# Optimization experiments

Hardware: AMD Instinct MI355X
Metric: run time of the kernel (lower is better)

## Reference

```python
import jax, jax.numpy as jnp
import numpy as np

NUM_RELATIONS = 16


def rgcn_conv(x, src, dst, etype, W, root, b):
    """PyG-style RGCNConv: per-relation mean aggregation + root weight + bias.

    x: [N, din]; W: [R, din, dout]; root: [din, dout]; b: [dout].
    """
    N, din = x.shape
    R = W.shape[0]
    E = src.shape[0]
    xe = x[src]                                   # [E, din] gather
    seg = etype * N + dst                          # combined (relation, dst) key
    sums = jax.ops.segment_sum(xe, seg, num_segments=R * N)        # [R*N, din]
    cnt = jax.ops.segment_sum(jnp.ones((E,), x.dtype), seg, num_segments=R * N)
    mean = (sums / jnp.maximum(cnt, 1.0)[:, None]).reshape(R, N, din)
    # mean-then-transform == PyG transform-then-mean (linearity)
    out = jnp.einsum('rnd,rde->ne', mean, W) + x @ root + b
    return out


def setup_inputs() -> dict:
    key = jax.random.key(0)
    ks = jax.random.split(key, 8)
    N, E, DIN, H, OUT, R = 40000, 640000, 386, 256, 2, NUM_RELATIONS
    x = jax.random.normal(ks[0], (N, DIN), dtype=jnp.float32)
    edge_index = jax.random.randint(ks[1], (2, E), 0, N, dtype=jnp.int64)
    edge_type = jax.random.randint(ks[2], (E,), 0, R, dtype=jnp.int64)
    s1 = 1.0 / np.sqrt(DIN)
    s2 = 1.0 / np.sqrt(H)
    W1 = jax.random.normal(ks[3], (R, DIN, H), dtype=jnp.float32) * s1
    root1 = jax.random.normal(ks[4], (DIN, H), dtype=jnp.float32) * s1
    b1 = jnp.zeros((H,), dtype=jnp.float32)
    W2 = jax.random.normal(ks[5], (R, H, OUT), dtype=jnp.float32) * s2
    root2 = jax.random.normal(ks[6], (H, OUT), dtype=jnp.float32) * s2
    b2 = jnp.zeros((OUT,), dtype=jnp.float32)
    return {"x": x, "edge_index": edge_index, "edge_type": edge_type,
            "W1": W1, "root1": root1, "b1": b1,
            "W2": W2, "root2": root2, "b2": b2}


def reference(x, edge_index, edge_type, W1, root1, b1, W2, root2, b2):
    src, dst = edge_index[0], edge_index[1]
    h = jax.nn.relu(rgcn_conv(x, src, dst, edge_type, W1, root1, b1))
    h = rgcn_conv(h, src, dst, edge_type, W2, root2, b2)
    return jnp.tanh(h)
```

## Files before the change

### kernel.cpp

```cpp
#include <hip/hip_runtime.h>
#include <cstdint>
#include <cstddef>

#define N_NODES 40000
#define DIN     386
#define H1      256
#define NREL    16
#define KPAD    416
#define MPAD    40064
#define NMT     313
#define NBREL   16
#define NCOL1   ((NREL + 1) * H1)
#define Y2C     (2 * NREL + 2)
#define N2PAD   48
#define LDB2    264
#define NWPR    625
#define ROWCAP  26112
#define NMTCP   208
#define NSB     40
#define NXB     8138
#define NB1B    7072
#define NB2B    48

typedef __attribute__((ext_vector_type(8))) short s8v;
typedef __attribute__((ext_vector_type(4))) float f4v;

__device__ __forceinline__ uint16_t f2h(float f) {
  _Float16 h = (_Float16)f;
  return *(uint16_t*)&h;
}
__device__ __forceinline__ float h2f(uint16_t u) {
  _Float16 h = *(_Float16*)&u;
  return (float)h;
}
__device__ __forceinline__ f4v mfma_f16(s8v a, s8v b, f4v c) {
  asm("v_mfma_f32_16x16x32_f16 %0, %1, %2, %0" : "+v"(c) : "v"(a), "v"(b));
  return c;
}
__device__ __forceinline__ void gload16(const uint16_t* g, const uint16_t* lds) {
  __builtin_amdgcn_global_load_lds(
      (const __attribute__((address_space(1))) unsigned int*)g,
      (__attribute__((address_space(3))) unsigned int*)lds, 16, 0, 0);
}

__global__ void k_count(const int* __restrict__ src, const int* __restrict__ dst,
                        const int* __restrict__ et, int* __restrict__ deg,
                        uint8_t* __restrict__ flagS, int* __restrict__ epos, int E) {
  int e = blockIdx.x * 256 + threadIdx.x;
  if (e < E) {
    epos[e] = atomicAdd(&deg[dst[e]], 1);
    flagS[et[e] * N_NODES + src[e]] = 1;
  }
}

__global__ void k_wcount(const uint8_t* __restrict__ flagS, int* __restrict__ wcnt) {
  int i = blockIdx.x * 256 + threadIdx.x;
  unsigned long long m = __ballot(flagS[i] != 0);
  if ((threadIdx.x & 63) == 0) wcnt[i >> 6] = (int)__popcll(m);
}

__global__ void k_scan1(const int* __restrict__ wcnt, int* __restrict__ wbase,
                        int* __restrict__ nsrc, const int* __restrict__ deg,
                        int* __restrict__ rowptr, int* __restrict__ bsum) {
  __shared__ int sd[1024];
  int t = threadIdx.x;
  if (blockIdx.x < NREL) {
    int r = blockIdx.x;
    int v = (t < NWPR) ? wcnt[r * NWPR + t] : 0;
    sd[t] = v;
    __syncthreads();
    for (int off = 1; off < 1024; off <<= 1) {
      int x = (t >= off) ? sd[t - off] : 0;
      __syncthreads();
      sd[t] += x;
      __syncthreads();
    }
    if (t < NWPR) wbase[r * NWPR + t] = sd[t] - v;
    if (t == NWPR - 1) nsrc[r] = sd[t];
  } else {
    int b = blockIdx.x - NREL;
    int i = b * 1024 + t;
    int v = (i < N_NODES) ? deg[i] : 0;
    sd[t] = v;
    __syncthreads();
    for (int off = 1; off < 1024; off <<= 1) {
      int x = (t >= off) ? sd[t - off] : 0;
      __syncthreads();
      sd[t] += x;
      __syncthreads();
    }
    if (i < N_NODES) rowptr[i + 1] = sd[t];
    if (t == 1023) bsum[b] = sd[t];
  }
}

__global__ void k_assign(const uint8_t* __restrict__ flagS,
                         const int* __restrict__ wbase,
                         int* __restrict__ posmap, int* __restrict__ srclist) {
  int i = blockIdx.x * 256 + threadIdx.x;
  int lane = threadIdx.x & 63;
  bool act = flagS[i] != 0;
  unsigned long long m = __ballot(act);
  if (act) {
    int pre = (int)__popcll(m & ((1ULL << lane) - 1));
    int p = wbase[i >> 6] + pre;
    int r = i / N_NODES, s = i - r * N_NODES;
    if (p < ROWCAP) {
      posmap[i] = p;
      srclist[r * ROWCAP + p] = s;
    } else {
      posmap[i] = ROWCAP - 1;
    }
  }
}

__global__ void k_s3(const int* __restrict__ bsum, int* __restrict__ rowptr) {
  __shared__ int s_off;
  int b = blockIdx.x, t = threadIdx.x;
  if (t < 64) {
    int lane = t;
    int v = (lane < NSB) ? bsum[lane] : 0;
    for (int o = 1; o < 64; o <<= 1) {
      int x = __shfl_up(v, o);
      if (lane >= o) v += x;
    }
    int off = (b == 0) ? 0 : __shfl(v, b - 1);
    if (lane == 0) s_off = off;
  }
  __syncthreads();
  int off = s_off;
  int i = b * 1024 + t;
  if (i < N_NODES && b > 0) rowptr[i + 1] += off;
  if (b == 0 && t == 0) rowptr[0] = 0;
}

__global__ void k_scatter(const int* __restrict__ src, const int* __restrict__ dst,
                          const int* __restrict__ et, const int* __restrict__ rowptr,
                          const int* __restrict__ epos, const int* __restrict__ posmap,
                          int* __restrict__ e_rp, int* __restrict__ e_rs, int E) {
  int e = blockIdx.x * 256 + threadIdx.x;
  if (e < E) {
    int d = dst[e], r = et[e], s = src[e];
    int idx = rowptr[d] + epos[e];
    e_rp[idx] = (r << 16) | posmap[r * N_NODES + s];
    e_rs[idx] = (r << 16) | s;
  }
}

__global__ void k_pack(const float* __restrict__ x, const float* __restrict__ W1,
                       const float* __restrict__ root1, const float* __restrict__ W2,
                       const float* __restrict__ root2, uint16_t* __restrict__ xh,
                       uint16_t* __restrict__ b1h, uint16_t* __restrict__ b2h) {
  int bb = blockIdx.x;
  int tid = threadIdx.x;
  if (bb < NXB) {
    long long i = (long long)bb * 256 + tid;
    if (i >= (long long)MPAD * (KPAD / 8)) return;
    int n = (int)(i / (KPAD / 8)), kv = (int)(i % (KPAD / 8));
    int k = kv * 8;
    uint4 o = {0u, 0u, 0u, 0u};
    if (n < N_NODES) {
      const float* xr = x + (long long)n * DIN;
      if (k + 8 <= DIN) {
        float2 p0 = *(const float2*)(xr + k);
        float2 p1 = *(const float2*)(xr + k + 2);
        float2 p2 = *(const float2*)(xr + k + 4);
        float2 p3 = *(const float2*)(xr + k + 6);
        o.x = (uint32_t)f2h(p0.x) | ((uint32_t)f2h(p0.y) << 16);
        o.y = (uint32_t)f2h(p1.x) | ((uint32_t)f2h(p1.y) << 16);
        o.z = (uint32_t)f2h(p2.x) | ((uint32_t)f2h(p2.y) << 16);
        o.w = (uint32_t)f2h(p3.x) | ((uint32_t)f2h(p3.y) << 16);
      } else if (k < DIN) {
        uint16_t t[8];
#pragma unroll
        for (int j = 0; j < 8; ++j) t[j] = (k + j < DIN) ? f2h(xr[k + j]) : 0;
        o.x = (uint32_t)t[0] | ((uint32_t)t[1] << 16);
        o.y = (uint32_t)t[2] | ((uint32_t)t[3] << 16);
        o.z = (uint32_t)t[4] | ((uint32_t)t[5] << 16);
        o.w = (uint32_t)t[6] | ((uint32_t)t[7] << 16);
      }
    }
    *(uint4*)(xh + (long long)n * KPAD + k) = o;
  } else if (bb < NXB + NB1B) {
    long long i = (long long)(bb - NXB) * 256 + tid;
    int c = (int)(i / KPAD), k = (int)(i % KPAD);
    float v = 0.0f;
    if (k < DIN) {
      if (c < NREL * H1) {
        int r = c >> 8, j = c & 255;
        v = W1[((long long)r * DIN + k) * H1 + j];
      } else {
        v = root1[(long long)k * H1 + (c - NREL * H1)];
      }
    }
    b1h[i] = f2h(v);
  } else {
    int i = (bb - NXB - NB1B) * 256 + tid;
    int c = i >> 8, k = i & 255;
    float v = 0.0f;
    if (c < 2 * NREL) { int r = c >> 1, j = c & 1; v = W2[(r * H1 + k) * 2 + j]; }
    else if (c < Y2C) v = root2[k * 2 + (c - 2 * NREL)];
    b2h[i] = f2h(v);
  }
}

__global__ __launch_bounds__(256) void k_gemm1(
    const uint16_t* __restrict__ A, const uint16_t* __restrict__ B,
    const uint16_t* __restrict__ Broot, uint16_t* __restrict__ C,
    uint16_t* __restrict__ h, int ldc, int nb, int jrel,
    const int* __restrict__ srclist, const int* __restrict__ nsrc, int r0) {
  __shared__ __align__(16) uint16_t sA[2][128 * 32];
  __shared__ __align__(16) uint16_t sB[2][256 * 32];
  int tid = threadIdx.x;
  int lane = tid & 63, w = tid >> 6;
  int wr = w >> 1, wcn = w & 1;

  int f = blockIdx.x;
  int xcd = f & 7, j = f >> 3;
  bool root = (j >= jrel);
  int mt, yt = 0, ns;
  const uint16_t* Bp;
  long long bn = 0;
  if (!root) {
    yt = j % nb;
    mt = (j / nb) * 8 + xcd;
    ns = nsrc[r0 + yt];
    if (ns > ROWCAP) ns = ROWCAP;
    Bp = B;
    bn = (long long)yt * 256;
  } else {
    mt = (j - jrel) * 8 + xcd;
    if (mt >= NMT) return;
    ns = N_NODES;
    Bp = Broot;
  }
  long long bm = (long long)mt * 128;
  if (bm >= ns) return;

  int lrow = lane & 15;
  int lko = (((lane >> 4) ^ ((lane >> 1) & 3)) * 8);

  int arow = tid >> 2;
  int skel = (((tid & 3) ^ ((tid >> 3) & 3)) * 8);

  long long rowA0, rowA1;
  if (!root) {
    const int* sl = srclist + (r0 + yt) * ROWCAP;
    int ia = (int)bm + arow, ib = ia + 64;
    rowA0 = sl[ia < ns ? ia : 0];
    rowA1 = sl[ib < ns ? ib : 0];
  } else {
    rowA0 = bm + arow;
    rowA1 = bm + arow + 64;
  }

  const uint16_t* gA0 = A + rowA0 * KPAD + skel;
  const uint16_t* gA1 = A + rowA1 * KPAD + skel;
  const uint16_t* gB0 = Bp + (bn + arow) * KPAD + skel;
  const uint16_t* gB1 = gB0 + (long long)64 * KPAD;
  const uint16_t* gB2 = gB0 + (long long)128 * KPAD;
  const uint16_t* gB3 = gB0 + (long long)192 * KPAD;

  f4v zero = {0.f, 0.f, 0.f, 0.f};
  f4v acc[4][8];
#pragma unroll
  for (int i = 0; i < 4; ++i)
#pragma unroll
    for (int jj = 0; jj < 8; ++jj) acc[i][jj] = zero;

  gload16(gA0, sA[0] + w * 512);
  gload16(gA1, sA[0] + 2048 + w * 512);
  gload16(gB0, sB[0] + w * 512);
  gload16(gB1, sB[0] + 2048 + w * 512);
  gload16(gB2, sB[0] + 4096 + w * 512);
  gload16(gB3, sB[0] + 6144 + w * 512);

  const int NIT = KPAD / 32;
  int cur = 0;
  for (int it = 0; it < NIT; ++it) {
    if (it + 1 < NIT) {
      int kk = (it + 1) * 32;
      int nxt = cur ^ 1;
      gload16(gA0 + kk, sA[nxt] + w * 512);
      gload16(gA1 + kk, sA[nxt] + 2048 + w * 512);
      gload16(gB0 + kk, sB[nxt] + w * 512);
      gload16(gB1 + kk, sB[nxt] + 2048 + w * 512);
      gload16(gB2 + kk, sB[nxt] + 4096 + w * 512);
      gload16(gB3 + kk, sB[nxt] + 6144 + w * 512);
      asm volatile("s_waitcnt vmcnt(6)" ::: "memory");
    } else {
      asm volatile("s_waitcnt vmcnt(0)" ::: "memory");
    }
    __builtin_amdgcn_s_barrier();

    const uint16_t* pA = sA[cur];
    const uint16_t* pB = sB[cur];
    s8v af[4];
#pragma unroll
    for (int mi = 0; mi < 4; ++mi)
      af[mi] = *(const s8v*)(pA + (wr * 64 + mi * 16 + lrow) * 32 + lko);
#pragma unroll
    for (int ni = 0; ni < 8; ++ni) {
      s8v bf = *(const s8v*)(pB + (wcn * 128 + ni * 16 + lrow) * 32 + lko);
#pragma unroll
      for (int mi = 0; mi < 4; ++mi)
        acc[mi][ni] = mfma_f16(af[mi], bf, acc[mi][ni]);
    }
    __builtin_amdgcn_s_barrier();
    cur ^= 1;
  }

  int rg = (lane >> 4) * 4;
  if (!root) {
#pragma unroll
    for (int mi = 0; mi < 4; ++mi) {
#pragma unroll
      for (int ni = 0; ni < 8; ++ni) {
        long long col = bn + wcn * 128 + ni * 16 + (lane & 15);
#pragma unroll
        for (int r2 = 0; r2 < 4; ++r2) {
          long long row = bm + wr * 64 + mi * 16 + rg + r2;
          C[row * ldc + col] = f2h(acc[mi][ni][r2]);
        }
      }
    }
  } else {
#pragma unroll
    for (int mi = 0; mi < 4; ++mi) {
#pragma unroll
      for (int ni = 0; ni < 8; ++ni) {
        int col = wcn * 128 + ni * 16 + (lane & 15);
#pragma unroll
        for (int r2 = 0; r2 < 4; ++r2) {
          long long row = bm + wr * 64 + mi * 16 + rg + r2;
          if (row < N_NODES) h[row * H1 + col] = f2h(acc[mi][ni][r2]);
        }
      }
    }
  }
}

__global__ __launch_bounds__(256) void k_agg1(
    const uint16_t* __restrict__ y1, const int* __restrict__ e_rp,
    const int* __restrict__ rowptr, uint16_t* __restrict__ h,
    const float* __restrict__ b1, int r0, int nb, int ldy, int fin) {
  int n = blockIdx.x * 4 + (threadIdx.x >> 6);
  int lane = threadIdx.x & 63;
  if (n >= N_NODES) return;
  int e0 = rowptr[n], e1 = rowptr[n + 1];
  int deg = e1 - e0;

  int mrp = (lane < deg) ? e_rp[e0 + lane] : -1;
  int myrel = mrp >> 16;
  int cmine = 0;
#pragma unroll
  for (int r = 0; r < 16; ++r) {
    unsigned long long m = __ballot(myrel == r);
    if (lane == r) cmine = (int)__popcll(m);
  }
  for (int base = e0 + 64; base < e1; base += 64) {
    int vv = (base + lane < e1) ? e_rp[base + lane] : -1;
    int rr = vv >> 16;
#pragma unroll
    for (int r = 0; r < 16; ++r) {
      unsigned long long m = __ballot(rr == r);
      if (lane == r) cmine += (int)__popcll(m);
    }
  }

  float4 acc = {0.f, 0.f, 0.f, 0.f};
  int dcap = deg <= 64 ? deg : 64;
  for (int j = 0; j < dcap; ++j) {
    int v = __shfl(mrp, j);
    int rel = v >> 16;
    int off = rel - r0;
    int cv = __shfl(cmine, rel & 15);
    if ((unsigned)off < (unsigned)nb) {
      int pos = v & 0xFFFF;
      float w = 1.0f / (float)cv;
      uint2 q = *(const uint2*)(y1 + (long long)pos * ldy + off * H1 + lane * 4);
      acc.x += w * h2f((uint16_t)q.x);
      acc.y += w * h2f((uint16_t)(q.x >> 16));
      acc.z += w * h2f((uint16_t)q.y);
      acc.w += w * h2f((uint16_t)(q.y >> 16));
    }
  }
  for (int e = e0 + 64; e < e1; ++e) {
    int v = e_rp[e];
    int rel = v >> 16;
    int off = rel - r0;
    int cv = __shfl(cmine, rel & 15);
    if ((unsigned)off < (unsigned)nb) {
      int pos = v & 0xFFFF;
      float w = 1.0f / (float)cv;
      uint2 q = *(const uint2*)(y1 + (long long)pos * ldy + off * H1 + lane * 4);
      acc.x += w * h2f((uint16_t)q.x);
      acc.y += w * h2f((uint16_t)(q.x >> 16));
      acc.z += w * h2f((uint16_t)q.y);
      acc.w += w * h2f((uint16_t)(q.y >> 16));
    }
  }

  uint16_t* hp = h + (long long)n * H1 + lane * 4;
  uint2 hv = *(const uint2*)hp;
  float o0 = h2f((uint16_t)hv.x) + acc.x;
  float o1 = h2f((uint16_t)(hv.x >> 16)) + acc.y;
  float o2 = h2f((uint16_t)hv.y) + acc.z;
  float o3 = h2f((uint16_t)(hv.y >> 16)) + acc.w;
  if (fin) {
    float4 bv = *(const float4*)(b1 + lane * 4);
    o0 += bv.x; o0 = o0 > 0.f ? o0 : 0.f;
    o1 += bv.y; o1 = o1 > 0.f ? o1 : 0.f;
    o2 += bv.z; o2 = o2 > 0.f ? o2 : 0.f;
    o3 += bv.w; o3 = o3 > 0.f ? o3 : 0.f;
  }
  uint2 o;
  o.x = (uint32_t)f2h(o0) | ((uint32_t)f2h(o1) << 16);
  o.y = (uint32_t)f2h(o2) | ((uint32_t)f2h(o3) << 16);
  *(uint2*)hp = o;
}

__global__ __launch_bounds__(256) void k_gemm2m(
    const uint16_t* __restrict__ h, const uint16_t* __restrict__ b2h,
    uint16_t* __restrict__ y2) {
  __shared__ __align__(16) uint16_t sB[N2PAD * LDB2];
  __shared__ __align__(16) uint16_t sA[128 * 32];
  int tid = threadIdx.x, lane = tid & 63, w = tid >> 6;
  long long bm = (long long)blockIdx.x * 128;

  for (int cid = tid; cid < N2PAD * 32; cid += 256) {
    int row = cid >> 5, off = cid & 31;
    *(uint4*)(&sB[row * LDB2 + off * 8]) = *(const uint4*)(b2h + row * H1 + off * 8);
  }

  f4v zero = {0.f, 0.f, 0.f, 0.f};
  f4v acc[2][3];
#pragma unroll
  for (int i = 0; i < 2; ++i)
#pragma unroll
    for (int j = 0; j < 3; ++j) acc[i][j] = zero;

  int lrow = lane & 15;
  int lko = (((lane >> 4) ^ ((lane >> 1) & 3)) * 8);
  int srow0 = w * 32 + (lane >> 2), srow1 = srow0 + 16;
  int skel = (((lane & 3) ^ ((lane >> 3) & 3)) * 8);

  for (int kk = 0; kk < H1; kk += 32) {
    gload16(h + (bm + srow0) * H1 + kk + skel, sA + w * 1024);
    gload16(h + (bm + srow1) * H1 + kk + skel, sA + w * 1024 + 512);
    __syncthreads();

    s8v ah[2];
#pragma unroll
    for (int mi = 0; mi < 2; ++mi)
      ah[mi] = *(const s8v*)(sA + (w * 32 + mi * 16 + lrow) * 32 + lko);
#pragma unroll
    for (int nj = 0; nj < 3; ++nj) {
      s8v bh = *(const s8v*)(&sB[(nj * 16 + lrow) * LDB2 + kk + ((lane >> 4) * 8)]);
#pragma unroll
      for (int mi = 0; mi < 2; ++mi)
        acc[mi][nj] = mfma_f16(ah[mi], bh, acc[mi][nj]);
    }
    __syncthreads();
  }
  int rg = (lane >> 4) * 4;
#pragma unroll
  for (int mi = 0; mi < 2; ++mi) {
#pragma unroll
    for (int nj = 0; nj < 3; ++nj) {
      int col = nj * 16 + (lane & 15);
      if (col < Y2C) {
#pragma unroll
        for (int r2 = 0; r2 < 4; ++r2) {
          long long row = bm + w * 32 + mi * 16 + rg + r2;
          if (row < N_NODES) y2[row * Y2C + col] = f2h(acc[mi][nj][r2]);
        }
      }
    }
  }
}

__global__ void k_agg2(const uint16_t* __restrict__ y2, const int* __restrict__ e_rs,
                       const int* __restrict__ rowptr, const float* __restrict__ b2,
                       float* __restrict__ out) {
  int n = blockIdx.x * 4 + (threadIdx.x >> 6);
  int lane = threadIdx.x & 63;
  if (n >= N_NODES) return;
  int e0 = rowptr[n], e1 = rowptr[n + 1];

  int v0 = (e0 + lane < e1) ? e_rs[e0 + lane] : -1;
  int rel0 = v0 >> 16;
  int cmine = 0;
#pragma unroll
  for (int r = 0; r < 16; ++r) {
    unsigned long long m = __ballot(rel0 == r);
    if (lane == r) cmine = (int)__popcll(m);
  }
  for (int base = e0 + 64; base < e1; base += 64) {
    int vv = (base + lane < e1) ? e_rs[base + lane] : -1;
    int rr = vv >> 16;
#pragma unroll
    for (int r = 0; r < 16; ++r) {
      unsigned long long m = __ballot(rr == r);
      if (lane == r) cmine += (int)__popcll(m);
    }
  }

  float a0 = 0.f, a1 = 0.f;
  {
    int cv = __shfl(cmine, rel0 & 15);
    if (v0 >= 0) {
      int s = v0 & 0xFFFF;
      float w = 1.0f / (float)cv;
      uint32_t q = *(const uint32_t*)(y2 + (long long)s * Y2C + rel0 * 2);
      a0 += w * h2f((uint16_t)q);
      a1 += w * h2f((uint16_t)(q >> 16));
    }
  }
  for (int base = e0 + 64; base < e1; base += 64) {
    int vv = (base + lane < e1) ? e_rs[base + lane] : -1;
    int rr = vv >> 16;
    int cv = __shfl(cmine, rr & 15);
    if (vv >= 0) {
      int s = vv & 0xFFFF;
      float w = 1.0f / (float)cv;
      uint32_t q = *(const uint32_t*)(y2 + (long long)s * Y2C + rr * 2);
      a0 += w * h2f((uint16_t)q);
      a1 += w * h2f((uint16_t)(q >> 16));
    }
  }
#pragma unroll
  for (int off = 32; off > 0; off >>= 1) {
    a0 += __shfl_down(a0, off);
    a1 += __shfl_down(a1, off);
  }
  if (lane == 0) {
    uint32_t q = *(const uint32_t*)(y2 + (long long)n * Y2C + 2 * NREL);
    a0 += h2f((uint16_t)q) + b2[0];
    a1 += h2f((uint16_t)(q >> 16)) + b2[1];
    out[n * 2] = tanhf(a0);
    out[n * 2 + 1] = tanhf(a1);
  }
}

extern "C" void kernel_launch(void* const* d_in, const int* in_sizes, int n_in,
                              void* d_out, int out_size, void* d_ws, size_t ws_size,
                              hipStream_t stream) {
  const float* x     = (const float*)d_in[0];
  const int*   ei    = (const int*)d_in[1];
  const int*   et    = (const int*)d_in[2];
  const float* W1    = (const float*)d_in[3];
  const float* root1 = (const float*)d_in[4];
  const float* b1    = (const float*)d_in[5];
  const float* W2    = (const float*)d_in[6];
  const float* root2 = (const float*)d_in[7];
  const float* b2    = (const float*)d_in[8];
  const int E = in_sizes[2];
  const int* src = ei;
  const int* dst = ei + E;

  char* ws = (char*)d_ws;
  size_t off = 0;
  auto alloc = [&](size_t bytes) {
    size_t o = off; off += (bytes + 255) & ~(size_t)255; return o;
  };
  size_t o_deg  = alloc((size_t)(N_NODES + 1) * 4);
  size_t o_flag = alloc((size_t)NREL * N_NODES);
  size_t zero_bytes = off;
  size_t o_nsrc = alloc(64 * 4);
  size_t o_wcnt = alloc((size_t)NREL * NWPR * 4);
  size_t o_wbas = alloc((size_t)NREL * NWPR * 4);
  size_t o_h    = alloc((size_t)MPAD * H1 * 2);
  size_t o_rp   = alloc((size_t)(N_NODES + 1) * 4);
  size_t o_bsum = alloc(64 * 4);
  size_t o_erp  = alloc((size_t)E * 4);
  size_t o_ers  = alloc((size_t)E * 4);
  size_t o_slst = alloc((size_t)NREL * ROWCAP * 4);
  size_t o_xh   = alloc((size_t)MPAD * KPAD * 2);
  size_t o_b1h  = alloc((size_t)NCOL1 * KPAD * 2);
  size_t o_b2h  = alloc((size_t)N2PAD * H1 * 2);
  size_t o_y2   = alloc((size_t)N_NODES * Y2C * 2);
  size_t o_y1   = off;

  int*      deg  = (int*)(ws + o_deg);
  uint8_t*  flg  = (uint8_t*)(ws + o_flag);
  int*      nsrc = (int*)(ws + o_nsrc);
  int*      wcnt = (int*)(ws + o_wcnt);
  int*      wbas = (int*)(ws + o_wbas);
  uint16_t* h    = (uint16_t*)(ws + o_h);
  int*      rp   = (int*)(ws + o_rp);
  int*      bsum = (int*)(ws + o_bsum);
  int*      erp  = (int*)(ws + o_erp);
  int*      ers  = (int*)(ws + o_ers);
  int*      slst = (int*)(ws + o_slst);
  uint16_t* xh   = (uint16_t*)(ws + o_xh);
  uint16_t* b1h  = (uint16_t*)(ws + o_b1h);
  uint16_t* b2h  = (uint16_t*)(ws + o_b2h);
  uint16_t* y2   = (uint16_t*)(ws + o_y2);
  uint16_t* y1   = (uint16_t*)(ws + o_y1);
  int*      epin = (int*)(ws + o_y1);
  int*      pmap = (int*)(ws + o_y1 + (((size_t)E * 4 + 255) & ~(size_t)255));

  size_t per_block = (size_t)ROWCAP * H1 * 2;
  int G = 1;
  if (ws_size > o_y1 + per_block) {
    size_t g = (ws_size - o_y1) / per_block;
    G = (int)(g > (size_t)NBREL ? (size_t)NBREL : g);
  }
  int npass = (NBREL + G - 1) / G;
  int Gb = (NBREL + npass - 1) / npass;

  const int NCB = NREL * N_NODES / 256;
  const int JROOT = 40;

  hipMemsetAsync(ws, 0, zero_bytes, stream);
  k_count<<<(E + 255) / 256, 256, 0, stream>>>(src, dst, et, deg, flg, epin, E);
  k_wcount<<<NCB, 256, 0, stream>>>(flg, wcnt);
  k_scan1<<<NREL + NSB, 1024, 0, stream>>>(wcnt, wbas, nsrc, deg, rp, bsum);
  k_assign<<<NCB, 256, 0, stream>>>(flg, wbas, pmap, slst);
  k_s3<<<NSB, 1024, 0, stream>>>(bsum, rp);
  k_scatter<<<(E + 255) / 256, 256, 0, stream>>>(src, dst, et, rp, epin, pmap,
                                                 erp, ers, E);
  k_pack<<<NXB + NB1B + NB2B, 256, 0, stream>>>(x, W1, root1, W2, root2,
                                                xh, b1h, b2h);

  int r0 = 0;
  for (int p = 0; p < npass; ++p) {
    int nb = (NBREL - r0 < Gb) ? (NBREL - r0) : Gb;
    int jrel = (NMTCP / 8) * nb;
    int jroot = (p == 0) ? JROOT : 0;
    int nwg = 8 * (jrel + jroot);
    k_gemm1<<<nwg, 256, 0, stream>>>(xh, b1h + (size_t)r0 * H1 * KPAD,
                                     b1h + (size_t)NREL * H1 * KPAD, y1, h,
                                     nb * H1, nb, jrel, slst, nsrc, r0);
    k_agg1<<<(N_NODES + 3) / 4, 256, 0, stream>>>(y1, erp, rp, h, b1,
                                                  r0, nb, nb * H1,
                                                  (p == npass - 1) ? 1 : 0);
    r0 += nb;
  }
  k_gemm2m<<<MPAD / 128, 256, 0, stream>>>(h, b2h, y2);
  k_agg2<<<(N_NODES + 3) / 4, 256, 0, stream>>>(y2, ers, rp, b2,
                                                (float*)d_out);
  (void)n_in; (void)out_size;
}
```

Baseline: 362.0 us.

## Fuse preprocessing kernels, double-buffer layer-2 GEMM, raise MFMA wave priority

Folds the per-64-node flag counting into the scan kernel using vectorized popcount, and merges the position-assignment and rowptr offset kernels into one launch. This cuts two kernel launches and an intermediate buffer. The layer-2 GEMM now double-buffers its A tile so global loads overlap the MFMAs, and both GEMMs raise wave priority around the MFMA loops. These are several unrelated changes bundled together, and each is small relative to the large GEMM and aggregation kernels.

```diff
diff --git a/kernel.cpp b/kernel.cpp
--- a/kernel.cpp
+++ b/kernel.cpp
@@ -21,6 +21,7 @@
 #define NXB     8138
 #define NB1B    7072
 #define NB2B    48
+#define NCB4    625
 
 typedef __attribute__((ext_vector_type(8))) short s8v;
 typedef __attribute__((ext_vector_type(4))) float f4v;
@@ -53,20 +54,23 @@
   }
 }
 
-__global__ void k_wcount(const uint8_t* __restrict__ flagS, int* __restrict__ wcnt) {
-  int i = blockIdx.x * 256 + threadIdx.x;
-  unsigned long long m = __ballot(flagS[i] != 0);
-  if ((threadIdx.x & 63) == 0) wcnt[i >> 6] = (int)__popcll(m);
-}
-
-__global__ void k_scan1(const int* __restrict__ wcnt, int* __restrict__ wbase,
+__global__ void k_scan1(const uint8_t* __restrict__ flagS, int* __restrict__ wbase,
                         int* __restrict__ nsrc, const int* __restrict__ deg,
                         int* __restrict__ rowptr, int* __restrict__ bsum) {
   __shared__ int sd[1024];
   int t = threadIdx.x;
   if (blockIdx.x < NREL) {
     int r = blockIdx.x;
-    int v = (t < NWPR) ? wcnt[r * NWPR + t] : 0;
+    int v = 0;
+    if (t < NWPR) {
+      const uint4* p = (const uint4*)(flagS + (size_t)r * N_NODES + t * 64);
+#pragma unroll
+      for (int q = 0; q < 4; ++q) {
+        uint4 u = p[q];
+        v += __popc(u.x & 0x01010101u) + __popc(u.y & 0x01010101u) +
+             __popc(u.z & 0x01010101u) + __popc(u.w & 0x01010101u);
+      }
+    }
     sd[t] = v;
     __syncthreads();
     for (int off = 1; off < 1024; off <<= 1) {
@@ -94,44 +98,46 @@
   }
 }
 
-__global__ void k_assign(const uint8_t* __restrict__ flagS,
-                         const int* __restrict__ wbase,
-                         int* __restrict__ posmap, int* __restrict__ srclist) {
-  int i = blockIdx.x * 256 + threadIdx.x;
-  int lane = threadIdx.x & 63;
-  bool act = flagS[i] != 0;
-  unsigned long long m = __ballot(act);
-  if (act) {
-    int pre = (int)__popcll(m & ((1ULL << lane) - 1));
-    int p = wbase[i >> 6] + pre;
-    int r = i / N_NODES, s = i - r * N_NODES;
-    if (p < ROWCAP) {
-      posmap[i] = p;
-      srclist[r * ROWCAP + p] = s;
-    } else {
-      posmap[i] = ROWCAP - 1;
-    }
-  }
-}
-
-__global__ void k_s3(const int* __restrict__ bsum, int* __restrict__ rowptr) {
-  __shared__ int s_off;
-  int b = blockIdx.x, t = threadIdx.x;
-  if (t < 64) {
-    int lane = t;
-    int v = (lane < NSB) ? bsum[lane] : 0;
-    for (int o = 1; o < 64; o <<= 1) {
-      int x = __shfl_up(v, o);
-      if (lane >= o) v += x;
-    }
-    int off = (b == 0) ? 0 : __shfl(v, b - 1);
-    if (lane == 0) s_off = off;
-  }
-  __syncthreads();
-  int off = s_off;
-  int i = b * 1024 + t;
-  if (i < N_NODES && b > 0) rowptr[i + 1] += off;
-  if (b == 0 && t == 0) rowptr[0] = 0;
+__global__ void k_assign_s3(const uint8_t* __restrict__ flagS,
+                            const int* __restrict__ wbase,
+                            int* __restrict__ posmap, int* __restrict__ srclist,
+                            const int* __restrict__ bsum, int* __restrict__ rowptr) {
+  int t = threadIdx.x;
+  if (blockIdx.x < NCB4) {
+    int i = blockIdx.x * 1024 + t;
+    int lane = t & 63;
+    bool act = flagS[i] != 0;
+    unsigned long long m = __ballot(act);
+    if (act) {
+      int pre = (int)__popcll(m & ((1ULL << lane) - 1));
+      int p = wbase[i >> 6] + pre;
+      int r = i / N_NODES, s = i - r * N_NODES;
+      if (p < ROWCAP) {
+        posmap[i] = p;
+        srclist[r * ROWCAP + p] = s;
+      } else {
+        posmap[i] = ROWCAP - 1;
+      }
+    }
+  } else {
+    __shared__ int s_off;
+    int b = blockIdx.x - NCB4;
+    if (t < 64) {
+      int lane = t;
+      int v = (lane < NSB) ? bsum[lane] : 0;
+      for (int o = 1; o < 64; o <<= 1) {
+        int x = __shfl_up(v, o);
+        if (lane >= o) v += x;
+      }
+      int off = (b == 0) ? 0 : __shfl(v, b - 1);
+      if (lane == 0) s_off = off;
+    }
+    __syncthreads();
+    int off = s_off;
+    int i = b * 1024 + t;
+    if (i < N_NODES && b > 0) rowptr[i + 1] += off;
+    if (b == 0 && t == 0) rowptr[0] = 0;
+  }
 }
 
 __global__ void k_scatter(const int* __restrict__ src, const int* __restrict__ dst,
@@ -239,7 +245,6 @@
 
   int lrow = lane & 15;
   int lko = (((lane >> 4) ^ ((lane >> 1) & 3)) * 8);
-
   int arow = tid >> 2;
   int skel = (((tid & 3) ^ ((tid >> 3) & 3)) * 8);
 
@@ -299,6 +304,7 @@
 #pragma unroll
     for (int mi = 0; mi < 4; ++mi)
       af[mi] = *(const s8v*)(pA + (wr * 64 + mi * 16 + lrow) * 32 + lko);
+    __builtin_amdgcn_s_setprio(1);
 #pragma unroll
     for (int ni = 0; ni < 8; ++ni) {
       s8v bf = *(const s8v*)(pB + (wcn * 128 + ni * 16 + lrow) * 32 + lko);
@@ -306,6 +312,7 @@
       for (int mi = 0; mi < 4; ++mi)
         acc[mi][ni] = mfma_f16(af[mi], bf, acc[mi][ni]);
     }
+    __builtin_amdgcn_s_setprio(0);
     __builtin_amdgcn_s_barrier();
     cur ^= 1;
   }
@@ -424,36 +431,51 @@
     const uint16_t* __restrict__ h, const uint16_t* __restrict__ b2h,
     uint16_t* __restrict__ y2) {
   __shared__ __align__(16) uint16_t sB[N2PAD * LDB2];
-  __shared__ __align__(16) uint16_t sA[128 * 32];
+  __shared__ __align__(16) uint16_t sA[2][128 * 32];
   int tid = threadIdx.x, lane = tid & 63, w = tid >> 6;
   long long bm = (long long)blockIdx.x * 128;
-
-  for (int cid = tid; cid < N2PAD * 32; cid += 256) {
-    int row = cid >> 5, off = cid & 31;
-    *(uint4*)(&sB[row * LDB2 + off * 8]) = *(const uint4*)(b2h + row * H1 + off * 8);
-  }
-
-  f4v zero = {0.f, 0.f, 0.f, 0.f};
-  f4v acc[2][3];
-#pragma unroll
-  for (int i = 0; i < 2; ++i)
-#pragma unroll
-    for (int j = 0; j < 3; ++j) acc[i][j] = zero;
 
   int lrow = lane & 15;
   int lko = (((lane >> 4) ^ ((lane >> 1) & 3)) * 8);
   int srow0 = w * 32 + (lane >> 2), srow1 = srow0 + 16;
   int skel = (((lane & 3) ^ ((lane >> 3) & 3)) * 8);
 
-  for (int kk = 0; kk < H1; kk += 32) {
-    gload16(h + (bm + srow0) * H1 + kk + skel, sA + w * 1024);
-    gload16(h + (bm + srow1) * H1 + kk + skel, sA + w * 1024 + 512);
-    __syncthreads();
-
+  gload16(h + (bm + srow0) * H1 + skel, sA[0] + w * 1024);
+  gload16(h + (bm + srow1) * H1 + skel, sA[0] + w * 1024 + 512);
+
+  for (int cid = tid; cid < N2PAD * 32; cid += 256) {
+    int row = cid >> 5, off = cid & 31;
+    *(uint4*)(&sB[row * LDB2 + off * 8]) = *(const uint4*)(b2h + row * H1 + off * 8);
+  }
+  __syncthreads();
+
+  f4v zero = {0.f, 0.f, 0.f, 0.f};
+  f4v acc[2][3];
+#pragma unroll
+  for (int i = 0; i < 2; ++i)
+#pragma unroll
+    for (int j = 0; j < 3; ++j) acc[i][j] = zero;
+
+  const int NIT = H1 / 32;
+  int cur = 0;
+  for (int it = 0; it < NIT; ++it) {
+    if (it + 1 < NIT) {
+      int kk = (it + 1) * 32;
+      int nxt = cur ^ 1;
+      gload16(h + (bm + srow0) * H1 + kk + skel, sA[nxt] + w * 1024);
+      gload16(h + (bm + srow1) * H1 + kk + skel, sA[nxt] + w * 1024 + 512);
+      asm volatile("s_waitcnt vmcnt(2)" ::: "memory");
+    } else {
+      asm volatile("s_waitcnt vmcnt(0)" ::: "memory");
+    }
+    __builtin_amdgcn_s_barrier();
+
+    int kk = it * 32;
     s8v ah[2];
 #pragma unroll
     for (int mi = 0; mi < 2; ++mi)
-      ah[mi] = *(const s8v*)(sA + (w * 32 + mi * 16 + lrow) * 32 + lko);
+      ah[mi] = *(const s8v*)(sA[cur] + (w * 32 + mi * 16 + lrow) * 32 + lko);
+    __builtin_amdgcn_s_setprio(1);
 #pragma unroll
     for (int nj = 0; nj < 3; ++nj) {
       s8v bh = *(const s8v*)(&sB[(nj * 16 + lrow) * LDB2 + kk + ((lane >> 4) * 8)]);
@@ -461,7 +483,9 @@
       for (int mi = 0; mi < 2; ++mi)
         acc[mi][nj] = mfma_f16(ah[mi], bh, acc[mi][nj]);
     }
-    __syncthreads();
+    __builtin_amdgcn_s_setprio(0);
+    __builtin_amdgcn_s_barrier();
+    cur ^= 1;
   }
   int rg = (lane >> 4) * 4;
 #pragma unroll
@@ -568,7 +592,6 @@
   size_t o_flag = alloc((size_t)NREL * N_NODES);
   size_t zero_bytes = off;
   size_t o_nsrc = alloc(64 * 4);
-  size_t o_wcnt = alloc((size_t)NREL * NWPR * 4);
   size_t o_wbas = alloc((size_t)NREL * NWPR * 4);
   size_t o_h    = alloc((size_t)MPAD * H1 * 2);
   size_t o_rp   = alloc((size_t)(N_NODES + 1) * 4);
@@ -585,7 +608,6 @@
   int*      deg  = (int*)(ws + o_deg);
   uint8_t*  flg  = (uint8_t*)(ws + o_flag);
   int*      nsrc = (int*)(ws + o_nsrc);
-  int*      wcnt = (int*)(ws + o_wcnt);
   int*      wbas = (int*)(ws + o_wbas);
   uint16_t* h    = (uint16_t*)(ws + o_h);
   int*      rp   = (int*)(ws + o_rp);
@@ -610,15 +632,12 @@
   int npass = (NBREL + G - 1) / G;
   int Gb = (NBREL + npass - 1) / npass;
 
-  const int NCB = NREL * N_NODES / 256;
   const int JROOT = 40;
 
   hipMemsetAsync(ws, 0, zero_bytes, stream);
   k_count<<<(E + 255) / 256, 256, 0, stream>>>(src, dst, et, deg, flg, epin, E);
-  k_wcount<<<NCB, 256, 0, stream>>>(flg, wcnt);
-  k_scan1<<<NREL + NSB, 1024, 0, stream>>>(wcnt, wbas, nsrc, deg, rp, bsum);
-  k_assign<<<NCB, 256, 0, stream>>>(flg, wbas, pmap, slst);
-  k_s3<<<NSB, 1024, 0, stream>>>(bsum, rp);
+  k_scan1<<<NREL + NSB, 1024, 0, stream>>>(flg, wbas, nsrc, deg, rp, bsum);
+  k_assign_s3<<<NCB4 + NSB, 1024, 0, stream>>>(flg, wbas, pmap, slst, bsum, rp);
   k_scatter<<<(E + 255) / 256, 256, 0, stream>>>(src, dst, et, rp, epin, pmap,
                                                  erp, ers, E);
   k_pack<<<NXB + NB1B + NB2B, 256, 0, stream>>>(x, W1, root1, W2, root2,
```

Result: faster. 345.6 us (-4.5%).
